# Kernel tuning notes

Measured on AMD Instinct MI355X. Metric: run time of the kernel, lower is better.

## Reference

```python
import jax, jax.numpy as jnp
import numpy as np

N_PROBLEMS = 50000
N_HIDDEN = 128
B, T = 32, 1024


def setup_inputs() -> dict:
    key = jax.random.key(0)
    k1, k2, k3, k4, k5 = jax.random.split(key, 5)
    y = jax.random.uniform(k1, (B, T), dtype=jnp.float32)
    problem_seq = jax.random.randint(k2, (B, T), 0, N_PROBLEMS)
    embd_weight = jax.random.normal(k3, (N_PROBLEMS, N_HIDDEN), dtype=jnp.float32)
    lam_w = jax.random.normal(k4, (N_HIDDEN, 1), dtype=jnp.float32) * (1.0 / np.sqrt(N_HIDDEN))
    lam_b = jax.random.normal(k5, (1,), dtype=jnp.float32) * 0.01
    return {"y": y, "problem_seq": problem_seq, "embd_weight": embd_weight,
            "lam_w": lam_w, "lam_b": lam_b}


def reference(y, problem_seq, embd_weight, lam_w, lam_b):
    # x: [B, t, h] embedded problem sequence
    x = embd_weight[problem_seq]
    # cosine-similarity matrix between timesteps: [B, t, t]
    mag = jnp.linalg.norm(embd_weight, axis=1)[problem_seq]      # [B, t]
    denom = mag[:, :, None] * mag[:, None, :]                    # [B, t, t]
    sim = jnp.einsum('bth,bsh->bts', x, x) / denom
    sim = (sim + 1.0) * 0.5
    t = sim.shape[1]
    # strictly-lower-triangular causal mask (tril with diagonal=-1)
    mask = jnp.tril(jnp.ones((t, t), dtype=sim.dtype), k=-1)
    sim = sim * mask
    # reversed cumsum over key axis (time-since accumulation)
    delta_t = jax.lax.cumsum(sim, axis=2, reverse=True)
    # per-query decay rate lambda: [B, t, 1]
    lam = jnp.exp(x @ lam_w + lam_b)
    weight = sim * jnp.exp(-lam * delta_t)
    weight_normed = weight / (weight.sum(axis=2, keepdims=True) + 1e-6)
    yhat = jnp.einsum('bs,bts->bt', y, weight_normed)
    return jnp.clip(yhat, 0.01, 0.99)
```

## Files before the change

### kernel.cpp

```cpp
#include <hip/hip_runtime.h>
#include <math.h>

#define BB 32
#define TT 1024
#define HH 128

typedef __attribute__((ext_vector_type(8))) short short8;
typedef __attribute__((ext_vector_type(4))) float floatx4;

__device__ __forceinline__ unsigned short f2bf(float f) {
    unsigned u = __float_as_uint(f);
    u += 0x7fffu + ((u >> 16) & 1u);
    return (unsigned short)(u >> 16);
}

__global__ __launch_bounds__(256)
void gather_norm(const int* __restrict__ seq,
                 const float* __restrict__ embd,
                 const float* __restrict__ lam_w,
                 const float* __restrict__ lam_b,
                 unsigned short* __restrict__ xbf,
                 float* __restrict__ lam) {
    const int lane = threadIdx.x & 63;
    const int half = lane >> 5;
    const int l32  = lane & 31;
    const int row  = blockIdx.x * 8 + (threadIdx.x >> 6) * 2 + half;
    const int idx  = seq[row];
    float4 v = ((const float4*)(embd + (size_t)idx * HH))[l32];
    float4 w = ((const float4*)lam_w)[l32];
    float ss = v.x * v.x + v.y * v.y + v.z * v.z + v.w * v.w;
    float dw = v.x * w.x + v.y * w.y + v.z * w.z + v.w * w.w;
    #pragma unroll
    for (int off = 16; off > 0; off >>= 1) {
        ss += __shfl_xor(ss, off);
        dw += __shfl_xor(dw, off);
    }
    float inv = 1.0f / sqrtf(ss);
    unsigned b0 = f2bf(v.x * inv), b1 = f2bf(v.y * inv);
    unsigned b2 = f2bf(v.z * inv), b3 = f2bf(v.w * inv);
    uint2 o; o.x = b0 | (b1 << 16); o.y = b2 | (b3 << 16);
    ((uint2*)(xbf + (size_t)row * HH))[l32] = o;
    if (l32 == 0) lam[row] = expf(dw + lam_b[0]);
}

__global__ __launch_bounds__(256)
void sim_kernel(const unsigned short* __restrict__ xbf,
                const float* __restrict__ lam,
                const float* __restrict__ y,
                float* __restrict__ out) {
    const int b    = blockIdx.x & 31;
    const int tt   = 63 - (blockIdx.x >> 5);
    const int tid  = threadIdx.x;
    const int wave = tid >> 6;
    const int lane = tid & 63;
    const int tl   = lane & 15;
    const int quad = lane >> 4;

    const int t = tt * 16 + tl;
    const size_t rowbase = (size_t)b * TT;
    const float lam_t = lam[rowbase + t];
    const float* yb = y + rowbase;

    __shared__ float Wc[4][16], Yc[4][16], Tc[4][16];

    short8 bq[4];
    const short8* qrow = (const short8*)(xbf + (rowbase + t) * HH);
    #pragma unroll
    for (int kk = 0; kk < 4; kk++) bq[kk] = qrow[kk * 4 + quad];

    const int n    = tt + 1;
    const int base = n >> 2, rem = n & 3;
    const int cnt   = base + (wave < rem ? 1 : 0);
    const int start = wave * base + (wave < rem ? wave : rem);

    float wsum = 0.f, wy = 0.f, run = 0.f;

    const int nsb = (cnt + 3) >> 2;
    for (int sb = nsb - 1; sb >= 0; --sb) {
        float vv[4][4];
        float tT[4], hq[4];

        #pragma unroll
        for (int j = 0; j < 4; j++) {
            const int i = sb * 4 + j;
            float v0 = 0.f, v1 = 0.f, v2 = 0.f, v3 = 0.f;
            if (i < cnt) {
                const int s_base = (start + i) << 4;
                const short8* arow =
                    (const short8*)(xbf + (rowbase + s_base + tl) * HH);
                floatx4 acc = {0.f, 0.f, 0.f, 0.f};
                #pragma unroll
                for (int kk = 0; kk < 4; kk++) {
                    short8 af = arow[kk * 4 + quad];
                    acc = __builtin_amdgcn_mfma_f32_16x16x32_bf16(af, bq[kk], acc, 0, 0, 0);
                }
                const int s0g = s_base + quad * 4;
                v0 = (s0g + 0 < t) ? (acc[0] + 1.f) * 0.5f : 0.f;
                v1 = (s0g + 1 < t) ? (acc[1] + 1.f) * 0.5f : 0.f;
                v2 = (s0g + 2 < t) ? (acc[2] + 1.f) * 0.5f : 0.f;
                v3 = (s0g + 3 < t) ? (acc[3] + 1.f) * 0.5f : 0.f;
            }
            vv[j][0] = v0; vv[j][1] = v1; vv[j][2] = v2; vv[j][3] = v3;
            float ts = (v0 + v1) + (v2 + v3);
            float q0 = __shfl(ts, tl);
            float q1 = __shfl(ts, tl + 16);
            float q2 = __shfl(ts, tl + 32);
            float q3 = __shfl(ts, tl + 48);
            tT[j] = (q0 + q1) + (q2 + q3);
            hq[j] = (quad < 1 ? q1 : 0.f) + (quad < 2 ? q2 : 0.f) +
                    (quad < 3 ? q3 : 0.f);
        }

        float d3 = hq[3] + run;
        float d2 = hq[2] + tT[3] + run;
        float d1 = hq[1] + (tT[2] + tT[3]) + run;
        float d0 = hq[0] + (tT[1] + (tT[2] + tT[3])) + run;
        run += (tT[0] + tT[1]) + (tT[2] + tT[3]);
        float dbase[4] = {d0, d1, d2, d3};

        #pragma unroll
        for (int j = 0; j < 4; j++) {
            const int i = sb * 4 + j;
            if (i < cnt) {
                const int s_base = (start + i) << 4;
                float v0 = vv[j][0], v1 = vv[j][1], v2 = vv[j][2], v3 = vv[j][3];
                float suf3 = v3;
                float suf2 = v2 + suf3;
                float suf1 = v1 + suf2;
                float suf0 = v0 + suf1;
                float db = dbase[j];
                float4 yv = ((const float4*)(yb + s_base))[quad];
                float w0 = v0 * __expf(-lam_t * (suf0 + db));
                float w1 = v1 * __expf(-lam_t * (suf1 + db));
                float w2 = v2 * __expf(-lam_t * (suf2 + db));
                float w3 = v3 * __expf(-lam_t * (suf3 + db));
                wsum += (w0 + w1) + (w2 + w3);
                wy   += w0 * yv.x + w1 * yv.y + w2 * yv.z + w3 * yv.w;
            }
        }
    }

    float Wt = __shfl(wsum, tl) + __shfl(wsum, tl + 16) +
               __shfl(wsum, tl + 32) + __shfl(wsum, tl + 48);
    float Yt = __shfl(wy, tl) + __shfl(wy, tl + 16) +
               __shfl(wy, tl + 32) + __shfl(wy, tl + 48);
    if (quad == 0) {
        Wc[wave][tl] = Wt;
        Yc[wave][tl] = Yt;
        Tc[wave][tl] = run;
    }
    __syncthreads();

    if (tid < 16) {
        float lt = lam[rowbase + tt * 16 + tid];
        float A = 0.f, W = 0.f, Y = 0.f;
        #pragma unroll
        for (int c = 3; c >= 0; --c) {
            float sc = __expf(-lt * A);
            W += Wc[c][tid] * sc;
            Y += Yc[c][tid] * sc;
            A += Tc[c][tid];
        }
        float r = Y / (W + 1e-6f);
        out[rowbase + tt * 16 + tid] = fminf(fmaxf(r, 0.01f), 0.99f);
    }
}

extern "C" void kernel_launch(void* const* d_in, const int* in_sizes, int n_in,
                              void* d_out, int out_size, void* d_ws, size_t ws_size,
                              hipStream_t stream) {
    const float* y     = (const float*)d_in[0];
    const int*   seq   = (const int*)  d_in[1];
    const float* embd  = (const float*)d_in[2];
    const float* lam_w = (const float*)d_in[3];
    const float* lam_b = (const float*)d_in[4];
    float* out = (float*)d_out;

    unsigned short* xbf = (unsigned short*)d_ws;
    float* lam = (float*)(xbf + (size_t)BB * TT * HH);

    gather_norm<<<BB * TT / 8, 256, 0, stream>>>(seq, embd, lam_w, lam_b, xbf, lam);
    sim_kernel<<<BB * 64, 256, 0, stream>>>(xbf, lam, y, out);
}
```

Measured before the change: 117.4 us.

## Split causal key range into fixed 64-key chunks with separate merge kernel

The single sim kernel, where four waves each looped over a variable share of the key tiles, is replaced by a grid of one wave per (batch, query tile, 64-key chunk). Each wave computes partial weighted sums and its chunk total, and a new merge kernel combines the 16 chunks per query using the decay rescaling. This evens out the work imbalance of the causal triangle and exposes far more parallelism. The cost is an extra launch, roughly half the waves exiting right away on masked chunks, and partial results round-tripping through global memory.

```diff
diff --git a/kernel.cpp b/kernel.cpp
--- a/kernel.cpp
+++ b/kernel.cpp
@@ -44,100 +44,90 @@
 }
 
 __global__ __launch_bounds__(256)
-void sim_kernel(const unsigned short* __restrict__ xbf,
-                const float* __restrict__ lam,
-                const float* __restrict__ y,
-                float* __restrict__ out) {
-    const int b    = blockIdx.x & 31;
-    const int tt   = 63 - (blockIdx.x >> 5);
-    const int tid  = threadIdx.x;
-    const int wave = tid >> 6;
-    const int lane = tid & 63;
+void sim_part(const unsigned short* __restrict__ xbf,
+              const float* __restrict__ lam,
+              const float* __restrict__ y,
+              float* __restrict__ Wp,
+              float* __restrict__ Yp,
+              float* __restrict__ Tp) {
+    const int wid  = blockIdx.x * 4 + (threadIdx.x >> 6);
+    const int c    = wid & 15;
+    const int tt   = (wid >> 4) & 63;
+    const int b    = wid >> 10;
+    const int lane = threadIdx.x & 63;
     const int tl   = lane & 15;
     const int quad = lane >> 4;
+    const int pi   = wid * 16 + tl;
+
+    if (4 * c > tt) {
+        if (quad == 0) { Wp[pi] = 0.f; Yp[pi] = 0.f; Tp[pi] = 0.f; }
+        return;
+    }
 
     const int t = tt * 16 + tl;
     const size_t rowbase = (size_t)b * TT;
     const float lam_t = lam[rowbase + t];
     const float* yb = y + rowbase;
 
-    __shared__ float Wc[4][16], Yc[4][16], Tc[4][16];
-
     short8 bq[4];
     const short8* qrow = (const short8*)(xbf + (rowbase + t) * HH);
     #pragma unroll
     for (int kk = 0; kk < 4; kk++) bq[kk] = qrow[kk * 4 + quad];
 
-    const int n    = tt + 1;
-    const int base = n >> 2, rem = n & 3;
-    const int cnt   = base + (wave < rem ? 1 : 0);
-    const int start = wave * base + (wave < rem ? wave : rem);
+    float vv[4][4];
+    float tT[4], hq[4];
 
-    float wsum = 0.f, wy = 0.f, run = 0.f;
+    #pragma unroll
+    for (int j = 0; j < 4; j++) {
+        const int s_base = (c * 4 + j) << 4;
+        const short8* arow =
+            (const short8*)(xbf + (rowbase + s_base + tl) * HH);
+        floatx4 acc = {0.f, 0.f, 0.f, 0.f};
+        #pragma unroll
+        for (int kk = 0; kk < 4; kk++) {
+            short8 af = arow[kk * 4 + quad];
+            acc = __builtin_amdgcn_mfma_f32_16x16x32_bf16(af, bq[kk], acc, 0, 0, 0);
+        }
+        const int s0g = s_base + quad * 4;
+        float v0 = (s0g + 0 < t) ? (acc[0] + 1.f) * 0.5f : 0.f;
+        float v1 = (s0g + 1 < t) ? (acc[1] + 1.f) * 0.5f : 0.f;
+        float v2 = (s0g + 2 < t) ? (acc[2] + 1.f) * 0.5f : 0.f;
+        float v3 = (s0g + 3 < t) ? (acc[3] + 1.f) * 0.5f : 0.f;
+        vv[j][0] = v0; vv[j][1] = v1; vv[j][2] = v2; vv[j][3] = v3;
+        float ts = (v0 + v1) + (v2 + v3);
+        float q0 = __shfl(ts, tl);
+        float q1 = __shfl(ts, tl + 16);
+        float q2 = __shfl(ts, tl + 32);
+        float q3 = __shfl(ts, tl + 48);
+        tT[j] = (q0 + q1) + (q2 + q3);
+        hq[j] = (quad < 1 ? q1 : 0.f) + (quad < 2 ? q2 : 0.f) +
+                (quad < 3 ? q3 : 0.f);
+    }
 
-    const int nsb = (cnt + 3) >> 2;
-    for (int sb = nsb - 1; sb >= 0; --sb) {
-        float vv[4][4];
-        float tT[4], hq[4];
+    float d3 = hq[3];
+    float d2 = hq[2] + tT[3];
+    float d1 = hq[1] + (tT[2] + tT[3]);
+    float d0 = hq[0] + (tT[1] + (tT[2] + tT[3]));
+    float Ttot = (tT[0] + tT[1]) + (tT[2] + tT[3]);
+    float dbase[4] = {d0, d1, d2, d3};
 
-        #pragma unroll
-        for (int j = 0; j < 4; j++) {
-            const int i = sb * 4 + j;
-            float v0 = 0.f, v1 = 0.f, v2 = 0.f, v3 = 0.f;
-            if (i < cnt) {
-                const int s_base = (start + i) << 4;
-                const short8* arow =
-                    (const short8*)(xbf + (rowbase + s_base + tl) * HH);
-                floatx4 acc = {0.f, 0.f, 0.f, 0.f};
-                #pragma unroll
-                for (int kk = 0; kk < 4; kk++) {
-                    short8 af = arow[kk * 4 + quad];
-                    acc = __builtin_amdgcn_mfma_f32_16x16x32_bf16(af, bq[kk], acc, 0, 0, 0);
-                }
-                const int s0g = s_base + quad * 4;
-                v0 = (s0g + 0 < t) ? (acc[0] + 1.f) * 0.5f : 0.f;
-                v1 = (s0g + 1 < t) ? (acc[1] + 1.f) * 0.5f : 0.f;
-                v2 = (s0g + 2 < t) ? (acc[2] + 1.f) * 0.5f : 0.f;
-                v3 = (s0g + 3 < t) ? (acc[3] + 1.f) * 0.5f : 0.f;
-            }
-            vv[j][0] = v0; vv[j][1] = v1; vv[j][2] = v2; vv[j][3] = v3;
-            float ts = (v0 + v1) + (v2 + v3);
-            float q0 = __shfl(ts, tl);
-            float q1 = __shfl(ts, tl + 16);
-            float q2 = __shfl(ts, tl + 32);
-            float q3 = __shfl(ts, tl + 48);
-            tT[j] = (q0 + q1) + (q2 + q3);
-            hq[j] = (quad < 1 ? q1 : 0.f) + (quad < 2 ? q2 : 0.f) +
-                    (quad < 3 ? q3 : 0.f);
-        }
-
-        float d3 = hq[3] + run;
-        float d2 = hq[2] + tT[3] + run;
-        float d1 = hq[1] + (tT[2] + tT[3]) + run;
-        float d0 = hq[0] + (tT[1] + (tT[2] + tT[3])) + run;
-        run += (tT[0] + tT[1]) + (tT[2] + tT[3]);
-        float dbase[4] = {d0, d1, d2, d3};
-
-        #pragma unroll
-        for (int j = 0; j < 4; j++) {
-            const int i = sb * 4 + j;
-            if (i < cnt) {
-                const int s_base = (start + i) << 4;
-                float v0 = vv[j][0], v1 = vv[j][1], v2 = vv[j][2], v3 = vv[j][3];
-                float suf3 = v3;
-                float suf2 = v2 + suf3;
-                float suf1 = v1 + suf2;
-                float suf0 = v0 + suf1;
-                float db = dbase[j];
-                float4 yv = ((const float4*)(yb + s_base))[quad];
-                float w0 = v0 * __expf(-lam_t * (suf0 + db));
-                float w1 = v1 * __expf(-lam_t * (suf1 + db));
-                float w2 = v2 * __expf(-lam_t * (suf2 + db));
-                float w3 = v3 * __expf(-lam_t * (suf3 + db));
-                wsum += (w0 + w1) + (w2 + w3);
-                wy   += w0 * yv.x + w1 * yv.y + w2 * yv.z + w3 * yv.w;
-            }
-        }
+    float wsum = 0.f, wy = 0.f;
+    #pragma unroll
+    for (int j = 0; j < 4; j++) {
+        const int s_base = (c * 4 + j) << 4;
+        float v0 = vv[j][0], v1 = vv[j][1], v2 = vv[j][2], v3 = vv[j][3];
+        float suf3 = v3;
+        float suf2 = v2 + suf3;
+        float suf1 = v1 + suf2;
+        float suf0 = v0 + suf1;
+        float db = dbase[j];
+        float4 yv = ((const float4*)(yb + s_base))[quad];
+        float w0 = v0 * __expf(-lam_t * (suf0 + db));
+        float w1 = v1 * __expf(-lam_t * (suf1 + db));
+        float w2 = v2 * __expf(-lam_t * (suf2 + db));
+        float w3 = v3 * __expf(-lam_t * (suf3 + db));
+        wsum += (w0 + w1) + (w2 + w3);
+        wy   += w0 * yv.x + w1 * yv.y + w2 * yv.z + w3 * yv.w;
     }
 
     float Wt = __shfl(wsum, tl) + __shfl(wsum, tl + 16) +
@@ -145,25 +135,35 @@
     float Yt = __shfl(wy, tl) + __shfl(wy, tl + 16) +
                __shfl(wy, tl + 32) + __shfl(wy, tl + 48);
     if (quad == 0) {
-        Wc[wave][tl] = Wt;
-        Yc[wave][tl] = Yt;
-        Tc[wave][tl] = run;
+        Wp[pi] = Wt;
+        Yp[pi] = Yt;
+        Tp[pi] = Ttot;
     }
-    __syncthreads();
+}
 
-    if (tid < 16) {
-        float lt = lam[rowbase + tt * 16 + tid];
-        float A = 0.f, W = 0.f, Y = 0.f;
-        #pragma unroll
-        for (int c = 3; c >= 0; --c) {
-            float sc = __expf(-lt * A);
-            W += Wc[c][tid] * sc;
-            Y += Yc[c][tid] * sc;
-            A += Tc[c][tid];
-        }
-        float r = Y / (W + 1e-6f);
-        out[rowbase + tt * 16 + tid] = fminf(fmaxf(r, 0.01f), 0.99f);
+__global__ __launch_bounds__(256)
+void merge_kernel(const float* __restrict__ Wp,
+                  const float* __restrict__ Yp,
+                  const float* __restrict__ Tp,
+                  const float* __restrict__ lam,
+                  float* __restrict__ out) {
+    const int id = blockIdx.x * 256 + threadIdx.x;
+    const int tl = id & 15;
+    const int bt = id >> 4;
+    const int t  = (bt & 63) * 16 + tl;
+    const int b  = bt >> 6;
+    const float lt = lam[b * TT + t];
+    float A = 0.f, W = 0.f, Y = 0.f;
+    #pragma unroll
+    for (int c = 15; c >= 0; --c) {
+        const int pi = (bt * 16 + c) * 16 + tl;
+        float sc = __expf(-lt * A);
+        W += Wp[pi] * sc;
+        Y += Yp[pi] * sc;
+        A += Tp[pi];
     }
+    float r = Y / (W + 1e-6f);
+    out[b * TT + t] = fminf(fmaxf(r, 0.01f), 0.99f);
 }
 
 extern "C" void kernel_launch(void* const* d_in, const int* in_sizes, int n_in,
@@ -178,7 +178,11 @@
 
     unsigned short* xbf = (unsigned short*)d_ws;
     float* lam = (float*)(xbf + (size_t)BB * TT * HH);
+    float* Wp  = lam + BB * TT;
+    float* Yp  = Wp + 32768 * 16;
+    float* Tp  = Yp + 32768 * 16;
 
     gather_norm<<<BB * TT / 8, 256, 0, stream>>>(seq, embd, lam_w, lam_b, xbf, lam);
-    sim_kernel<<<BB * 64, 256, 0, stream>>>(xbf, lam, y, out);
+    sim_part<<<32768 / 4, 256, 0, stream>>>(xbf, lam, y, Wp, Yp, Tp);
+    merge_kernel<<<BB * TT / 256, 256, 0, stream>>>(Wp, Yp, Tp, lam, out);
 }
```

After: 158.0 us. +34.5%, slower.

## Process two query tiles per block to reuse key fragments across MFMAs

Applied to the files above, without the earlier changes.

Each block now handles 32 query rows (two 16-row tiles) instead of 16, so every loaded key fragment feeds two MFMAs, halving key-row global loads per query. The per-tile suffix-sum decay is restructured into local tile weights that are later rescaled with a single exp factor, replacing the earlier two-pass dbase approach with an online scaling scheme. The grid halves to 1024 blocks, which reduces parallelism and adds register pressure; launch bounds are set to 4 blocks per CU.

```diff
diff --git a/kernel.cpp b/kernel.cpp
--- a/kernel.cpp
+++ b/kernel.cpp
@@ -43,126 +43,155 @@
     if (l32 == 0) lam[row] = expf(dw + lam_b[0]);
 }
 
-__global__ __launch_bounds__(256)
-void sim_kernel(const unsigned short* __restrict__ xbf,
-                const float* __restrict__ lam,
-                const float* __restrict__ y,
-                float* __restrict__ out) {
+__device__ __forceinline__ void tile_part(const floatx4& acc, int s0, int t,
+                                          float lmt, const float4& yv,
+                                          float& S, float& W, float& Y) {
+    float v0 = (s0 + 0 < t) ? (acc[0] + 1.f) * 0.5f : 0.f;
+    float v1 = (s0 + 1 < t) ? (acc[1] + 1.f) * 0.5f : 0.f;
+    float v2 = (s0 + 2 < t) ? (acc[2] + 1.f) * 0.5f : 0.f;
+    float v3 = (s0 + 3 < t) ? (acc[3] + 1.f) * 0.5f : 0.f;
+    float suf3 = v3;
+    float suf2 = v2 + suf3;
+    float suf1 = v1 + suf2;
+    float suf0 = v0 + suf1;
+    float e0 = __expf(-lmt * suf0);
+    float e1 = __expf(-lmt * suf1);
+    float e2 = __expf(-lmt * suf2);
+    float e3 = __expf(-lmt * suf3);
+    float w0 = v0 * e0, w1 = v1 * e1, w2 = v2 * e2, w3 = v3 * e3;
+    S = suf0;
+    W = (w0 + w1) + (w2 + w3);
+    Y = (w0 * yv.x + w1 * yv.y) + (w2 * yv.z + w3 * yv.w);
+}
+
+__device__ __forceinline__ void resolve(float S, float W, float Y, float lmt,
+                                        int tl, int quad,
+                                        float& above, float& wl, float& yl) {
+    float q0 = __shfl(S, tl);
+    float q1 = __shfl(S, tl + 16);
+    float q2 = __shfl(S, tl + 32);
+    float q3 = __shfl(S, tl + 48);
+    float tT = (q0 + q1) + (q2 + q3);
+    float hq = (quad < 1 ? q1 : 0.f) + (quad < 2 ? q2 : 0.f) +
+               (quad < 3 ? q3 : 0.f);
+    float sc = __expf(-lmt * (above + hq));
+    wl += W * sc;
+    yl += Y * sc;
+    above += tT;
+}
+
+__global__ __launch_bounds__(256, 4)
+void sim_fused(const unsigned short* __restrict__ xbf,
+               const float* __restrict__ lam,
+               const float* __restrict__ y,
+               float* __restrict__ out) {
     const int b    = blockIdx.x & 31;
-    const int tt   = 63 - (blockIdx.x >> 5);
+    const int u    = 31 - (blockIdx.x >> 5);
     const int tid  = threadIdx.x;
-    const int wave = tid >> 6;
+    const int w    = tid >> 6;
     const int lane = tid & 63;
     const int tl   = lane & 15;
     const int quad = lane >> 4;
 
-    const int t = tt * 16 + tl;
     const size_t rowbase = (size_t)b * TT;
-    const float lam_t = lam[rowbase + t];
+    const int t0 = u * 32 + tl;
+    const int t1 = t0 + 16;
+    const float lam0 = lam[rowbase + t0];
+    const float lam1 = lam[rowbase + t1];
     const float* yb = y + rowbase;
 
-    __shared__ float Wc[4][16], Yc[4][16], Tc[4][16];
-
-    short8 bq[4];
-    const short8* qrow = (const short8*)(xbf + (rowbase + t) * HH);
+    __shared__ float Wc[4][2][16], Yc[4][2][16], Tc[4][2][16];
+
+    short8 bq0[4], bq1[4];
+    const short8* q0r = (const short8*)(xbf + (rowbase + t0) * HH);
+    const short8* q1r = (const short8*)(xbf + (rowbase + t1) * HH);
     #pragma unroll
-    for (int kk = 0; kk < 4; kk++) bq[kk] = qrow[kk * 4 + quad];
-
-    const int n    = tt + 1;
-    const int base = n >> 2, rem = n & 3;
-    const int cnt   = base + (wave < rem ? 1 : 0);
-    const int start = wave * base + (wave < rem ? wave : rem);
-
-    float wsum = 0.f, wy = 0.f, run = 0.f;
-
-    const int nsb = (cnt + 3) >> 2;
+    for (int kk = 0; kk < 4; kk++) {
+        bq0[kk] = q0r[kk * 4 + quad];
+        bq1[kk] = q1r[kk * 4 + quad];
+    }
+
+    const int nst = 2 * u + 2;
+    const int qn = nst >> 2, rem = nst & 3;
+    const int cnt   = qn + (w < rem ? 1 : 0);
+    const int start = w * qn + (w < rem ? w : rem);
+
+    float wl0 = 0.f, yl0 = 0.f, above0 = 0.f;
+    float wl1 = 0.f, yl1 = 0.f, above1 = 0.f;
+
+    const int nsb = (cnt + 1) >> 1;
     for (int sb = nsb - 1; sb >= 0; --sb) {
-        float vv[4][4];
-        float tT[4], hq[4];
-
+        const int jA = start + 2 * sb;
+        const int jB = jA + 1;
+        const bool vB = (2 * sb + 1) < cnt;
+        const int sbaseA = jA << 4;
+        const int sbaseB = vB ? (jB << 4) : 0;
+
+        const short8* arA = (const short8*)(xbf + (rowbase + sbaseA + tl) * HH);
+        const short8* arB = (const short8*)(xbf + (rowbase + sbaseB + tl) * HH);
+        short8 afA[4], afB[4];
         #pragma unroll
-        for (int j = 0; j < 4; j++) {
-            const int i = sb * 4 + j;
-            float v0 = 0.f, v1 = 0.f, v2 = 0.f, v3 = 0.f;
-            if (i < cnt) {
-                const int s_base = (start + i) << 4;
-                const short8* arow =
-                    (const short8*)(xbf + (rowbase + s_base + tl) * HH);
-                floatx4 acc = {0.f, 0.f, 0.f, 0.f};
-                #pragma unroll
-                for (int kk = 0; kk < 4; kk++) {
-                    short8 af = arow[kk * 4 + quad];
-                    acc = __builtin_amdgcn_mfma_f32_16x16x32_bf16(af, bq[kk], acc, 0, 0, 0);
-                }
-                const int s0g = s_base + quad * 4;
-                v0 = (s0g + 0 < t) ? (acc[0] + 1.f) * 0.5f : 0.f;
-                v1 = (s0g + 1 < t) ? (acc[1] + 1.f) * 0.5f : 0.f;
-                v2 = (s0g + 2 < t) ? (acc[2] + 1.f) * 0.5f : 0.f;
-                v3 = (s0g + 3 < t) ? (acc[3] + 1.f) * 0.5f : 0.f;
-            }
-            vv[j][0] = v0; vv[j][1] = v1; vv[j][2] = v2; vv[j][3] = v3;
-            float ts = (v0 + v1) + (v2 + v3);
-            float q0 = __shfl(ts, tl);
-            float q1 = __shfl(ts, tl + 16);
-            float q2 = __shfl(ts, tl + 32);
-            float q3 = __shfl(ts, tl + 48);
-            tT[j] = (q0 + q1) + (q2 + q3);
-            hq[j] = (quad < 1 ? q1 : 0.f) + (quad < 2 ? q2 : 0.f) +
-                    (quad < 3 ? q3 : 0.f);
+        for (int kk = 0; kk < 4; kk++) {
+            afA[kk] = arA[kk * 4 + quad];
+            afB[kk] = arB[kk * 4 + quad];
         }
-
-        float d3 = hq[3] + run;
-        float d2 = hq[2] + tT[3] + run;
-        float d1 = hq[1] + (tT[2] + tT[3]) + run;
-        float d0 = hq[0] + (tT[1] + (tT[2] + tT[3])) + run;
-        run += (tT[0] + tT[1]) + (tT[2] + tT[3]);
-        float dbase[4] = {d0, d1, d2, d3};
-
+        float4 yvA = ((const float4*)(yb + sbaseA))[quad];
+        float4 yvB = ((const float4*)(yb + sbaseB))[quad];
+
+        floatx4 aA0 = {0,0,0,0}, aA1 = {0,0,0,0};
+        floatx4 aB0 = {0,0,0,0}, aB1 = {0,0,0,0};
         #pragma unroll
-        for (int j = 0; j < 4; j++) {
-            const int i = sb * 4 + j;
-            if (i < cnt) {
-                const int s_base = (start + i) << 4;
-                float v0 = vv[j][0], v1 = vv[j][1], v2 = vv[j][2], v3 = vv[j][3];
-                float suf3 = v3;
-                float suf2 = v2 + suf3;
-                float suf1 = v1 + suf2;
-                float suf0 = v0 + suf1;
-                float db = dbase[j];
-                float4 yv = ((const float4*)(yb + s_base))[quad];
-                float w0 = v0 * __expf(-lam_t * (suf0 + db));
-                float w1 = v1 * __expf(-lam_t * (suf1 + db));
-                float w2 = v2 * __expf(-lam_t * (suf2 + db));
-                float w3 = v3 * __expf(-lam_t * (suf3 + db));
-                wsum += (w0 + w1) + (w2 + w3);
-                wy   += w0 * yv.x + w1 * yv.y + w2 * yv.z + w3 * yv.w;
-            }
+        for (int kk = 0; kk < 4; kk++) {
+            aA0 = __builtin_amdgcn_mfma_f32_16x16x32_bf16(afA[kk], bq0[kk], aA0, 0, 0, 0);
+            aA1 = __builtin_amdgcn_mfma_f32_16x16x32_bf16(afA[kk], bq1[kk], aA1, 0, 0, 0);
+            aB0 = __builtin_amdgcn_mfma_f32_16x16x32_bf16(afB[kk], bq0[kk], aB0, 0, 0, 0);
+            aB1 = __builtin_amdgcn_mfma_f32_16x16x32_bf16(afB[kk], bq1[kk], aB1, 0, 0, 0);
         }
-    }
-
-    float Wt = __shfl(wsum, tl) + __shfl(wsum, tl + 16) +
-               __shfl(wsum, tl + 32) + __shfl(wsum, tl + 48);
-    float Yt = __shfl(wy, tl) + __shfl(wy, tl + 16) +
-               __shfl(wy, tl + 32) + __shfl(wy, tl + 48);
+
+        const int s0A = sbaseA + quad * 4;
+        const int s0B = vB ? (sbaseB + quad * 4) : 0x40000000;
+
+        float SB0, WB0, YB0, SB1, WB1, YB1;
+        float SA0, WA0, YA0, SA1, WA1, YA1;
+        tile_part(aB0, s0B, t0, lam0, yvB, SB0, WB0, YB0);
+        tile_part(aB1, s0B, t1, lam1, yvB, SB1, WB1, YB1);
+        tile_part(aA0, s0A, t0, lam0, yvA, SA0, WA0, YA0);
+        tile_part(aA1, s0A, t1, lam1, yvA, SA1, WA1, YA1);
+
+        resolve(SB0, WB0, YB0, lam0, tl, quad, above0, wl0, yl0);
+        resolve(SB1, WB1, YB1, lam1, tl, quad, above1, wl1, yl1);
+        resolve(SA0, WA0, YA0, lam0, tl, quad, above0, wl0, yl0);
+        resolve(SA1, WA1, YA1, lam1, tl, quad, above1, wl1, yl1);
+    }
+
+    float Wt0 = __shfl(wl0, tl) + __shfl(wl0, tl + 16) +
+                __shfl(wl0, tl + 32) + __shfl(wl0, tl + 48);
+    float Yt0 = __shfl(yl0, tl) + __shfl(yl0, tl + 16) +
+                __shfl(yl0, tl + 32) + __shfl(yl0, tl + 48);
+    float Wt1 = __shfl(wl1, tl) + __shfl(wl1, tl + 16) +
+                __shfl(wl1, tl + 32) + __shfl(wl1, tl + 48);
+    float Yt1 = __shfl(yl1, tl) + __shfl(yl1, tl + 16) +
+                __shfl(yl1, tl + 32) + __shfl(yl1, tl + 48);
     if (quad == 0) {
-        Wc[wave][tl] = Wt;
-        Yc[wave][tl] = Yt;
-        Tc[wave][tl] = run;
+        Wc[w][0][tl] = Wt0; Yc[w][0][tl] = Yt0; Tc[w][0][tl] = above0;
+        Wc[w][1][tl] = Wt1; Yc[w][1][tl] = Yt1; Tc[w][1][tl] = above1;
     }
     __syncthreads();
 
-    if (tid < 16) {
-        float lt = lam[rowbase + tt * 16 + tid];
+    if (tid < 32) {
+        const int g = tid >> 4, l = tid & 15;
+        const int t = u * 32 + g * 16 + l;
+        const float lt = lam[rowbase + t];
         float A = 0.f, W = 0.f, Y = 0.f;
         #pragma unroll
-        for (int c = 3; c >= 0; --c) {
+        for (int ww = 3; ww >= 0; --ww) {
             float sc = __expf(-lt * A);
-            W += Wc[c][tid] * sc;
-            Y += Yc[c][tid] * sc;
-            A += Tc[c][tid];
+            W += Wc[ww][g][l] * sc;
+            Y += Yc[ww][g][l] * sc;
+            A += Tc[ww][g][l];
         }
         float r = Y / (W + 1e-6f);
-        out[rowbase + tt * 16 + tid] = fminf(fmaxf(r, 0.01f), 0.99f);
+        out[rowbase + t] = fminf(fmaxf(r, 0.01f), 0.99f);
     }
 }
 
@@ -180,5 +209,5 @@
     float* lam = (float*)(xbf + (size_t)BB * TT * HH);
 
     gather_norm<<<BB * TT / 8, 256, 0, stream>>>(seq, embd, lam_w, lam_b, xbf, lam);
-    sim_kernel<<<BB * 64, 256, 0, stream>>>(xbf, lam, y, out);
-}
+    sim_fused<<<BB * 32, 256, 0, stream>>>(xbf, lam, y, out);
+}
```

After: 104.6 us. -10.9%, faster.
